# Performance work log

Hardware: AMD Instinct MI355X
Metric: run time of the kernel (lower is better)

## Reference

```python
import jax, jax.numpy as jnp
import numpy as np

ALPHA = 0.005
SCALE = 0.001
DELTA = 0.1
MAX_ITER = 50
EARLY = True


def setup_inputs() -> dict:
    key = jax.random.key(0)
    k1, k2, k3 = jax.random.split(key, 3)
    B, S, M, N = 32, 8, 512, 512
    x = jax.random.uniform(k1, (B, S, N), dtype=jnp.float32)
    A = jax.random.normal(k2, (B, S, M, N), dtype=jnp.float32) * 0.1
    b = jax.random.uniform(k3, (B, S, M), dtype=jnp.float32)
    return {"x": x, "A": A, "b": b}


def reference(x, A, b):
    # x: [B,S,N] primal iterate; A: [B,S,M,N] constraint matrices; b: [B,S,M]
    B, S = b.shape[0], b.shape[1]
    active0 = jnp.ones((B, S), dtype=bool)

    def body(carry, _):
        x_, active, stopped = carry
        # torch loop runs an iteration only while any(active) and not early-stopped
        run = jnp.any(active) & (~stopped)
        # Ax - b, clamped at 0 -> per-constraint violation
        Ax = jnp.einsum('bsn,bsmn->bsm', x_, A)          # [B,S,M]
        viol = jnp.clip(Ax - b, 0.0)
        new_active = jnp.sum(viol, axis=-1) >= DELTA      # ~(total < delta)
        stop_early = jnp.asarray(EARLY) & (~jnp.any(new_active))
        g = jnp.einsum('bsm,bsmn->bsn', viol, A)          # penalty gradient [B,S,N]
        lr = ALPHA / (1.0 + SCALE * g)
        x_upd = jnp.where(new_active[..., None], x_ - lr * g, x_)
        x_upd = jnp.clip(x_upd, 0.0)                      # clamp applied even to inactive rows
        # early stop happens BEFORE the update/clamp in the torch code
        x_new = jnp.where(stop_early, x_, x_upd)
        x_out = jnp.where(run, x_new, x_)
        active_out = jnp.where(run, new_active, active)
        stopped_out = stopped | (run & stop_early)
        return (x_out, active_out, stopped_out), None

    # torch: break when count > max_iter after increment -> up to max_iter+1 updates
    init = (x, active0, jnp.array(False))
    (x_final, _, _), _ = jax.lax.scan(body, init, None, length=MAX_ITER + 1)
    return x_final
```

## Files before the change

kernel.cpp:

```cpp
#include <hip/hip_runtime.h>

#define ALPHA 0.005f
#define SCALE 0.001f
#define DELTA 0.1f
#define MAXIT 51

constexpr int N = 512;
constexpr int M = 512;
constexpr int NTHREADS = 1024;
constexpr int NWAVES = NTHREADS / 64;
constexpr int MPW = M / NWAVES;
constexpr int NROWS = 256;
constexpr size_t WS_NEEDED = (size_t)NROWS * M * N * 2;

template<int CTRL>
__device__ __forceinline__ float dpp_mov(float v) {
    return __int_as_float(__builtin_amdgcn_update_dpp(
        0, __float_as_int(v), CTRL, 0xF, 0xF, true));
}

__device__ __forceinline__ float wave_sum_u(float d) {
    d += dpp_mov<0x111>(d);
    d += dpp_mov<0x112>(d);
    d += dpp_mov<0x114>(d);
    d += dpp_mov<0x118>(d);
    d += dpp_mov<0x142>(d);
    d += dpp_mov<0x143>(d);
    return __int_as_float(__builtin_amdgcn_readlane(__float_as_int(d), 63));
}

__device__ __forceinline__ float dot8(const float4& a, const float4& c,
                                      const float4& xa, const float4& xb) {
    return a.x*xa.x + a.y*xa.y + a.z*xa.z + a.w*xa.w
         + c.x*xb.x + c.y*xb.y + c.z*xb.z + c.w*xb.w;
}

__device__ __forceinline__ unsigned pack2_bf16(float f0, float f1) {
    unsigned a = __float_as_uint(f0); a += 0x7fffu + ((a >> 16) & 1u);
    unsigned b = __float_as_uint(f1); b += 0x7fffu + ((b >> 16) & 1u);
    return (a >> 16) | (b & 0xffff0000u);
}
__device__ __forceinline__ float bflo(unsigned u) { return __uint_as_float(u << 16); }
__device__ __forceinline__ float bfhi(unsigned u) { return __uint_as_float(u & 0xffff0000u); }

__device__ __forceinline__ void unpack4(uint2 u, float4& f) {
    f.x = bflo(u.x); f.y = bfhi(u.x); f.z = bflo(u.y); f.w = bfhi(u.y);
}

__global__ __launch_bounds__(NTHREADS, 4)
void lva_bf16_kernel(const float* __restrict__ x_in,
                     const float* __restrict__ A,
                     const float* __restrict__ bvec,
                     float* __restrict__ x_out,
                     unsigned short* __restrict__ wsA)
{
    __shared__ float b_lds[M];
    __shared__ float g_lds[2 * NWAVES * N];
    __shared__ float sv_lds[2 * NWAVES];
    __shared__ int bc_active;

    const int tid  = threadIdx.x;
    const int lane = tid & 63;
    const int w    = tid >> 6;
    const int r    = blockIdx.x;

    if (tid < M) b_lds[tid] = bvec[(size_t)r * M + tid];

    const int n0 = lane * 4;
    const int n1 = 256 + lane * 4;

    const float* xrow = x_in + (size_t)r * N;
    float4 xa = *(const float4*)(xrow + n0);
    float4 xb = *(const float4*)(xrow + n1);

    const float* Ablk = A + (size_t)r * M * N + (size_t)w * N;
    unsigned short* Wblk = wsA + (size_t)r * M * N + (size_t)w * N;

    __syncthreads();

    bool alive = true;

    {
        float4 ga = make_float4(0.f, 0.f, 0.f, 0.f);
        float4 gb = make_float4(0.f, 0.f, 0.f, 0.f);
        float sviol = 0.f;

        #pragma unroll 1
        for (int kk = 0; kk < MPW; kk += 4) {
            const float* p0 = Ablk + (size_t)(kk + 0) * (16 * N);
            const float* p1 = Ablk + (size_t)(kk + 1) * (16 * N);
            const float* p2 = Ablk + (size_t)(kk + 2) * (16 * N);
            const float* p3 = Ablk + (size_t)(kk + 3) * (16 * N);
            float4 a0 = *(const float4*)(p0 + n0), c0 = *(const float4*)(p0 + n1);
            float4 a1 = *(const float4*)(p1 + n0), c1 = *(const float4*)(p1 + n1);
            float4 a2 = *(const float4*)(p2 + n0), c2 = *(const float4*)(p2 + n1);
            float4 a3 = *(const float4*)(p3 + n0), c3 = *(const float4*)(p3 + n1);
            {
                unsigned short* q0 = Wblk + (size_t)(kk + 0) * (16 * N);
                unsigned short* q1 = Wblk + (size_t)(kk + 1) * (16 * N);
                unsigned short* q2 = Wblk + (size_t)(kk + 2) * (16 * N);
                unsigned short* q3 = Wblk + (size_t)(kk + 3) * (16 * N);
                *(uint2*)(q0 + n0) = make_uint2(pack2_bf16(a0.x, a0.y), pack2_bf16(a0.z, a0.w));
                *(uint2*)(q0 + n1) = make_uint2(pack2_bf16(c0.x, c0.y), pack2_bf16(c0.z, c0.w));
                *(uint2*)(q1 + n0) = make_uint2(pack2_bf16(a1.x, a1.y), pack2_bf16(a1.z, a1.w));
                *(uint2*)(q1 + n1) = make_uint2(pack2_bf16(c1.x, c1.y), pack2_bf16(c1.z, c1.w));
                *(uint2*)(q2 + n0) = make_uint2(pack2_bf16(a2.x, a2.y), pack2_bf16(a2.z, a2.w));
                *(uint2*)(q2 + n1) = make_uint2(pack2_bf16(c2.x, c2.y), pack2_bf16(c2.z, c2.w));
                *(uint2*)(q3 + n0) = make_uint2(pack2_bf16(a3.x, a3.y), pack2_bf16(a3.z, a3.w));
                *(uint2*)(q3 + n1) = make_uint2(pack2_bf16(c3.x, c3.y), pack2_bf16(c3.z, c3.w));
            }
            float bb0 = b_lds[w + 16 * (kk + 0)];
            float bb1 = b_lds[w + 16 * (kk + 1)];
            float bb2 = b_lds[w + 16 * (kk + 2)];
            float bb3 = b_lds[w + 16 * (kk + 3)];
            float d0 = wave_sum_u(dot8(a0, c0, xa, xb));
            float d1 = wave_sum_u(dot8(a1, c1, xa, xb));
            float d2 = wave_sum_u(dot8(a2, c2, xa, xb));
            float d3 = wave_sum_u(dot8(a3, c3, xa, xb));
            float v0 = fmaxf(d0 - bb0, 0.f);
            float v1 = fmaxf(d1 - bb1, 0.f);
            float v2 = fmaxf(d2 - bb2, 0.f);
            float v3 = fmaxf(d3 - bb3, 0.f);
            sviol += v0 + v1 + v2 + v3;
            ga.x += v0*a0.x + v1*a1.x + v2*a2.x + v3*a3.x;
            ga.y += v0*a0.y + v1*a1.y + v2*a2.y + v3*a3.y;
            ga.z += v0*a0.z + v1*a1.z + v2*a2.z + v3*a3.z;
            ga.w += v0*a0.w + v1*a1.w + v2*a2.w + v3*a3.w;
            gb.x += v0*c0.x + v1*c1.x + v2*c2.x + v3*c3.x;
            gb.y += v0*c0.y + v1*c1.y + v2*c2.y + v3*c3.y;
            gb.z += v0*c0.z + v1*c1.z + v2*c2.z + v3*c3.z;
            gb.w += v0*c0.w + v1*c1.w + v2*c2.w + v3*c3.w;
        }

        if (lane == 0) sv_lds[w] = sviol;
        *(float4*)(&g_lds[w * N + n0]) = ga;
        *(float4*)(&g_lds[w * N + n1]) = gb;
        __syncthreads();
        if (tid == 0) {
            float s = 0.f;
            #pragma unroll
            for (int i = 0; i < NWAVES; ++i) s += sv_lds[i];
            bc_active = (s >= DELTA) ? 1 : 0;
        }
        if (tid < N) {
            float s = 0.f;
            #pragma unroll
            for (int i = 0; i < NWAVES; ++i) s += g_lds[i * N + tid];
            g_lds[tid] = s;
        }
        __syncthreads();
        if (!bc_active) {
            alive = false;
        } else {
            float4 gfa = *(const float4*)(&g_lds[n0]);
            float4 gfb = *(const float4*)(&g_lds[n1]);
            xa.x = fmaxf(xa.x - (ALPHA / (1.f + SCALE*gfa.x)) * gfa.x, 0.f);
            xa.y = fmaxf(xa.y - (ALPHA / (1.f + SCALE*gfa.y)) * gfa.y, 0.f);
            xa.z = fmaxf(xa.z - (ALPHA / (1.f + SCALE*gfa.z)) * gfa.z, 0.f);
            xa.w = fmaxf(xa.w - (ALPHA / (1.f + SCALE*gfa.w)) * gfa.w, 0.f);
            xb.x = fmaxf(xb.x - (ALPHA / (1.f + SCALE*gfb.x)) * gfb.x, 0.f);
            xb.y = fmaxf(xb.y - (ALPHA / (1.f + SCALE*gfb.y)) * gfb.y, 0.f);
            xb.z = fmaxf(xb.z - (ALPHA / (1.f + SCALE*gfb.z)) * gfb.z, 0.f);
            xb.w = fmaxf(xb.w - (ALPHA / (1.f + SCALE*gfb.w)) * gfb.w, 0.f);
        }
    }

    const int h = lane >> 5;
    const int s = lane & 31;
    __syncthreads();
    if (w == 0) {
        *(float4*)(&g_lds[n0]) = xa;
        *(float4*)(&g_lds[n1]) = xb;
    }
    __syncthreads();
    float4 xf0 = *(const float4*)(&g_lds[  0 + s * 4]);
    float4 xf1 = *(const float4*)(&g_lds[128 + s * 4]);
    float4 xf2 = *(const float4*)(&g_lds[256 + s * 4]);
    float4 xf3 = *(const float4*)(&g_lds[384 + s * 4]);
    __syncthreads();

    if (alive) {
        const uint2* Wp = (const uint2*)(wsA + (size_t)r * M * N)
                          + (w + 16 * h) * 128 + s;
        const int mb = w + 16 * h;

        uint2 c0, c1, c2, c3, p0, p1, p2, p3;

        #define LOADG(b0, b1, b2, b3, Gn) do {  \
            b0 = Wp[(Gn) * 4096];               \
            b1 = Wp[(Gn) * 4096 + 32];          \
            b2 = Wp[(Gn) * 4096 + 64];          \
            b3 = Wp[(Gn) * 4096 + 96];          \
        } while (0)

        #define COMPUTE(b0, b1, b2, b3, G) do {                               \
            float4 f0, f1, f2, f3;                                            \
            unpack4(b0, f0); unpack4(b1, f1);                                 \
            unpack4(b2, f2); unpack4(b3, f3);                                 \
            float d = f0.x*xf0.x + f0.y*xf0.y + f0.z*xf0.z + f0.w*xf0.w       \
                    + f1.x*xf1.x + f1.y*xf1.y + f1.z*xf1.z + f1.w*xf1.w       \
                    + f2.x*xf2.x + f2.y*xf2.y + f2.z*xf2.z + f2.w*xf2.w       \
                    + f3.x*xf3.x + f3.y*xf3.y + f3.z*xf3.z + f3.w*xf3.w;      \
            d += dpp_mov<0xB1>(d);            \
            d += dpp_mov<0x4E>(d);            \
            d += dpp_mov<0x141>(d);           \
            d += dpp_mov<0x140>(d);           \
            d += __int_as_float(__builtin_amdgcn_ds_swizzle(                  \
                     __float_as_int(d), 0x401F));        \
            float v = fmaxf(d - b_lds[mb + 32 * (G)], 0.f);                   \
            sviol += v;                                                       \
            g0.x += v*f0.x; g0.y += v*f0.y; g0.z += v*f0.z; g0.w += v*f0.w;   \
            g1.x += v*f1.x; g1.y += v*f1.y; g1.z += v*f1.z; g1.w += v*f1.w;   \
            g2.x += v*f2.x; g2.y += v*f2.y; g2.z += v*f2.z; g2.w += v*f2.w;   \
            g3.x += v*f3.x; g3.y += v*f3.y; g3.z += v*f3.z; g3.w += v*f3.w;   \
        } while (0)

        LOADG(c0, c1, c2, c3, 0);

        for (int t = 1; t < MAXIT; ++t) {
            float4 g0 = make_float4(0.f, 0.f, 0.f, 0.f);
            float4 g1 = make_float4(0.f, 0.f, 0.f, 0.f);
            float4 g2 = make_float4(0.f, 0.f, 0.f, 0.f);
            float4 g3 = make_float4(0.f, 0.f, 0.f, 0.f);
            float sviol = 0.f;

            #pragma unroll 1
            for (int G = 0; G < 16; G += 2) {
                LOADG(p0, p1, p2, p3, G + 1);
                COMPUTE(c0, c1, c2, c3, G);
                LOADG(c0, c1, c2, c3, (G + 2) & 15);
                COMPUTE(p0, p1, p2, p3, G + 1);
            }

            if (s == 0) sv_lds[2 * w + h] = sviol;
            {
                const int gbase = (2 * w + h) * N + s * 4;
                *(float4*)(&g_lds[gbase +   0]) = g0;
                *(float4*)(&g_lds[gbase + 128]) = g1;
                *(float4*)(&g_lds[gbase + 256]) = g2;
                *(float4*)(&g_lds[gbase + 384]) = g3;
            }
            __syncthreads();
            if (tid == 0) {
                float sacc = 0.f;
                #pragma unroll
                for (int i = 0; i < 2 * NWAVES; ++i) sacc += sv_lds[i];
                bc_active = (sacc >= DELTA) ? 1 : 0;
            }
            if (tid < N) {
                float sacc = 0.f;
                #pragma unroll
                for (int i = 0; i < 2 * NWAVES; ++i) sacc += g_lds[i * N + tid];
                g_lds[tid] = sacc;
            }
            __syncthreads();
            if (!bc_active) break;

            float4 q0 = *(const float4*)(&g_lds[  0 + s * 4]);
            float4 q1 = *(const float4*)(&g_lds[128 + s * 4]);
            float4 q2 = *(const float4*)(&g_lds[256 + s * 4]);
            float4 q3 = *(const float4*)(&g_lds[384 + s * 4]);
            xf0.x = fmaxf(xf0.x - (ALPHA / (1.f + SCALE*q0.x)) * q0.x, 0.f);
            xf0.y = fmaxf(xf0.y - (ALPHA / (1.f + SCALE*q0.y)) * q0.y, 0.f);
            xf0.z = fmaxf(xf0.z - (ALPHA / (1.f + SCALE*q0.z)) * q0.z, 0.f);
            xf0.w = fmaxf(xf0.w - (ALPHA / (1.f + SCALE*q0.w)) * q0.w, 0.f);
            xf1.x = fmaxf(xf1.x - (ALPHA / (1.f + SCALE*q1.x)) * q1.x, 0.f);
            xf1.y = fmaxf(xf1.y - (ALPHA / (1.f + SCALE*q1.y)) * q1.y, 0.f);
            xf1.z = fmaxf(xf1.z - (ALPHA / (1.f + SCALE*q1.z)) * q1.z, 0.f);
            xf1.w = fmaxf(xf1.w - (ALPHA / (1.f + SCALE*q1.w)) * q1.w, 0.f);
            xf2.x = fmaxf(xf2.x - (ALPHA / (1.f + SCALE*q2.x)) * q2.x, 0.f);
            xf2.y = fmaxf(xf2.y - (ALPHA / (1.f + SCALE*q2.y)) * q2.y, 0.f);
            xf2.z = fmaxf(xf2.z - (ALPHA / (1.f + SCALE*q2.z)) * q2.z, 0.f);
            xf2.w = fmaxf(xf2.w - (ALPHA / (1.f + SCALE*q2.w)) * q2.w, 0.f);
            xf3.x = fmaxf(xf3.x - (ALPHA / (1.f + SCALE*q3.x)) * q3.x, 0.f);
            xf3.y = fmaxf(xf3.y - (ALPHA / (1.f + SCALE*q3.y)) * q3.y, 0.f);
            xf3.z = fmaxf(xf3.z - (ALPHA / (1.f + SCALE*q3.z)) * q3.z, 0.f);
            xf3.w = fmaxf(xf3.w - (ALPHA / (1.f + SCALE*q3.w)) * q3.w, 0.f);
            __syncthreads();
        }
        #undef LOADG
        #undef COMPUTE
    }

    if (w == 0 && h == 0) {
        float* orow = x_out + (size_t)r * N + s * 4;
        *(float4*)(orow +   0) = xf0;
        *(float4*)(orow + 128) = xf1;
        *(float4*)(orow + 256) = xf2;
        *(float4*)(orow + 384) = xf3;
    }
}

__global__ __launch_bounds__(NTHREADS, 4)
void lva_kernel(const float* __restrict__ x_in,
                const float* __restrict__ A,
                const float* __restrict__ bvec,
                float* __restrict__ x_out)
{
    __shared__ float b_lds[M];
    __shared__ float g_lds[NWAVES * N];
    __shared__ float sv_lds[NWAVES];
    __shared__ int bc_active;

    const int tid  = threadIdx.x;
    const int lane = tid & 63;
    const int w    = tid >> 6;
    const int r    = blockIdx.x;

    if (tid < M) b_lds[tid] = bvec[(size_t)r * M + tid];

    const int n0 = lane * 4;
    const int n1 = 256 + lane * 4;

    const float* xrow = x_in + (size_t)r * N;
    float4 xa = *(const float4*)(xrow + n0);
    float4 xb = *(const float4*)(xrow + n1);

    const float* Ablk = A + (size_t)r * M * N + (size_t)w * N;

    __syncthreads();

    for (int t = 0; t < MAXIT; ++t) {
        float4 ga = make_float4(0.f, 0.f, 0.f, 0.f);
        float4 gb = make_float4(0.f, 0.f, 0.f, 0.f);
        float sviol = 0.f;

        #pragma unroll 1
        for (int kk = 0; kk < MPW; kk += 4) {
            const float* p0 = Ablk + (size_t)(kk + 0) * (16 * N);
            const float* p1 = Ablk + (size_t)(kk + 1) * (16 * N);
            const float* p2 = Ablk + (size_t)(kk + 2) * (16 * N);
            const float* p3 = Ablk + (size_t)(kk + 3) * (16 * N);
            float4 a0 = *(const float4*)(p0 + n0), c0 = *(const float4*)(p0 + n1);
            float4 a1 = *(const float4*)(p1 + n0), c1 = *(const float4*)(p1 + n1);
            float4 a2 = *(const float4*)(p2 + n0), c2 = *(const float4*)(p2 + n1);
            float4 a3 = *(const float4*)(p3 + n0), c3 = *(const float4*)(p3 + n1);
            float bb0 = b_lds[w + 16 * (kk + 0)];
            float bb1 = b_lds[w + 16 * (kk + 1)];
            float bb2 = b_lds[w + 16 * (kk + 2)];
            float bb3 = b_lds[w + 16 * (kk + 3)];
            float d0 = wave_sum_u(dot8(a0, c0, xa, xb));
            float d1 = wave_sum_u(dot8(a1, c1, xa, xb));
            float d2 = wave_sum_u(dot8(a2, c2, xa, xb));
            float d3 = wave_sum_u(dot8(a3, c3, xa, xb));
            float v0 = fmaxf(d0 - bb0, 0.f);
            float v1 = fmaxf(d1 - bb1, 0.f);
            float v2 = fmaxf(d2 - bb2, 0.f);
            float v3 = fmaxf(d3 - bb3, 0.f);
            sviol += v0 + v1 + v2 + v3;
            ga.x += v0*a0.x + v1*a1.x + v2*a2.x + v3*a3.x;
            ga.y += v0*a0.y + v1*a1.y + v2*a2.y + v3*a3.y;
            ga.z += v0*a0.z + v1*a1.z + v2*a2.z + v3*a3.z;
            ga.w += v0*a0.w + v1*a1.w + v2*a2.w + v3*a3.w;
            gb.x += v0*c0.x + v1*c1.x + v2*c2.x + v3*c3.x;
            gb.y += v0*c0.y + v1*c1.y + v2*c2.y + v3*c3.y;
            gb.z += v0*c0.z + v1*c1.z + v2*c2.z + v3*c3.z;
            gb.w += v0*c0.w + v1*c1.w + v2*c2.w + v3*c3.w;
        }

        if (lane == 0) sv_lds[w] = sviol;
        *(float4*)(&g_lds[w * N + n0]) = ga;
        *(float4*)(&g_lds[w * N + n1]) = gb;
        __syncthreads();
        if (tid == 0) {
            float sacc = 0.f;
            #pragma unroll
            for (int i = 0; i < NWAVES; ++i) sacc += sv_lds[i];
            bc_active = (sacc >= DELTA) ? 1 : 0;
        }
        if (tid < N) {
            float sacc = 0.f;
            #pragma unroll
            for (int i = 0; i < NWAVES; ++i) sacc += g_lds[i * N + tid];
            g_lds[tid] = sacc;
        }
        __syncthreads();
        if (!bc_active) break;

        float4 gfa = *(const float4*)(&g_lds[n0]);
        float4 gfb = *(const float4*)(&g_lds[n1]);
        xa.x = fmaxf(xa.x - (ALPHA / (1.f + SCALE*gfa.x)) * gfa.x, 0.f);
        xa.y = fmaxf(xa.y - (ALPHA / (1.f + SCALE*gfa.y)) * gfa.y, 0.f);
        xa.z = fmaxf(xa.z - (ALPHA / (1.f + SCALE*gfa.z)) * gfa.z, 0.f);
        xa.w = fmaxf(xa.w - (ALPHA / (1.f + SCALE*gfa.w)) * gfa.w, 0.f);
        xb.x = fmaxf(xb.x - (ALPHA / (1.f + SCALE*gfb.x)) * gfb.x, 0.f);
        xb.y = fmaxf(xb.y - (ALPHA / (1.f + SCALE*gfb.y)) * gfb.y, 0.f);
        xb.z = fmaxf(xb.z - (ALPHA / (1.f + SCALE*gfb.z)) * gfb.z, 0.f);
        xb.w = fmaxf(xb.w - (ALPHA / (1.f + SCALE*gfb.w)) * gfb.w, 0.f);
        __syncthreads();
    }

    float* orow = x_out + (size_t)r * N;
    if (w == 0) {
        *(float4*)(orow + n0) = xa;
        *(float4*)(orow + n1) = xb;
    }
}

extern "C" void kernel_launch(void* const* d_in, const int* in_sizes, int n_in,
                              void* d_out, int out_size, void* d_ws, size_t ws_size,
                              hipStream_t stream)
{
    const float* x  = (const float*)d_in[0];
    const float* A  = (const float*)d_in[1];
    const float* b  = (const float*)d_in[2];
    float* out      = (float*)d_out;

    if (ws_size >= WS_NEEDED) {
        lva_bf16_kernel<<<dim3(NROWS), dim3(NTHREADS), 0, stream>>>(
            x, A, b, out, (unsigned short*)d_ws);
    } else {
        lva_kernel<<<dim3(NROWS), dim3(NTHREADS), 0, stream>>>(x, A, b, out);
    }
}
```

Measured before the change: 1.323 ms.

## Cache tail rows of bf16 A in LDS and widen iteration loads

The last 96 constraint rows of each block's bf16 copy of A now live in shared memory instead of the global workspace, so each iteration reads 13 of 16 row groups from global and 3 from LDS. The per-lane layout moves to 8 contiguous elements so rows load as uint4 instead of uint2. The loop is fully unrolled with a 4-deep register prefetch that crosses iterations. The two half-wave gradient partials are merged with ds_bpermute before the block reduction, halving the g_lds reduction work. The aim is less global and L2 traffic and latency per iteration, at the cost of about 96KB of LDS and more registers, which may reduce occupancy.

```diff
diff --git a/kernel.cpp b/kernel.cpp
--- a/kernel.cpp
+++ b/kernel.cpp
@@ -12,6 +12,9 @@
 constexpr int MPW = M / NWAVES;
 constexpr int NROWS = 256;
 constexpr size_t WS_NEEDED = (size_t)NROWS * M * N * 2;
+
+constexpr int CACHE_M0 = 416;
+constexpr int CACHE_KK0 = 26;
 
 template<int CTRL>
 __device__ __forceinline__ float dpp_mov(float v) {
@@ -43,10 +46,6 @@
 __device__ __forceinline__ float bflo(unsigned u) { return __uint_as_float(u << 16); }
 __device__ __forceinline__ float bfhi(unsigned u) { return __uint_as_float(u & 0xffff0000u); }
 
-__device__ __forceinline__ void unpack4(uint2 u, float4& f) {
-    f.x = bflo(u.x); f.y = bfhi(u.x); f.z = bflo(u.y); f.w = bfhi(u.y);
-}
-
 __global__ __launch_bounds__(NTHREADS, 4)
 void lva_bf16_kernel(const float* __restrict__ x_in,
                      const float* __restrict__ A,
@@ -54,10 +53,11 @@
                      float* __restrict__ x_out,
                      unsigned short* __restrict__ wsA)
 {
-    __shared__ float b_lds[M];
-    __shared__ float g_lds[2 * NWAVES * N];
-    __shared__ float sv_lds[2 * NWAVES];
+    __shared__ __align__(16) float b_lds[M];
+    __shared__ __align__(16) float g_lds[NWAVES * N];
+    __shared__ float sv_lds[NWAVES];
     __shared__ int bc_active;
+    __shared__ __align__(16) uint2 A_lds[96 * 128];
 
     const int tid  = threadIdx.x;
     const int lane = tid & 63;
@@ -84,6 +84,22 @@
         float4 ga = make_float4(0.f, 0.f, 0.f, 0.f);
         float4 gb = make_float4(0.f, 0.f, 0.f, 0.f);
         float sviol = 0.f;
+
+        #define STROW(j, aj, cj) do {                                               \
+            if (kk + (j) >= CACHE_KK0) {                                            \
+                const int rl = w + 16 * (kk + (j)) - CACHE_M0;                      \
+                A_lds[rl * 128 + lane]      = make_uint2(pack2_bf16(aj.x, aj.y),    \
+                                                         pack2_bf16(aj.z, aj.w));   \
+                A_lds[rl * 128 + 64 + lane] = make_uint2(pack2_bf16(cj.x, cj.y),    \
+                                                         pack2_bf16(cj.z, cj.w));   \
+            } else {                                                                \
+                unsigned short* q = Wblk + (size_t)(kk + (j)) * (16 * N);           \
+                *(uint2*)(q + n0) = make_uint2(pack2_bf16(aj.x, aj.y),              \
+                                               pack2_bf16(aj.z, aj.w));             \
+                *(uint2*)(q + n1) = make_uint2(pack2_bf16(cj.x, cj.y),              \
+                                               pack2_bf16(cj.z, cj.w));             \
+            }                                                                       \
+        } while (0)
 
         #pragma unroll 1
         for (int kk = 0; kk < MPW; kk += 4) {
@@ -95,20 +111,7 @@
             float4 a1 = *(const float4*)(p1 + n0), c1 = *(const float4*)(p1 + n1);
             float4 a2 = *(const float4*)(p2 + n0), c2 = *(const float4*)(p2 + n1);
             float4 a3 = *(const float4*)(p3 + n0), c3 = *(const float4*)(p3 + n1);
-            {
-                unsigned short* q0 = Wblk + (size_t)(kk + 0) * (16 * N);
-                unsigned short* q1 = Wblk + (size_t)(kk + 1) * (16 * N);
-                unsigned short* q2 = Wblk + (size_t)(kk + 2) * (16 * N);
-                unsigned short* q3 = Wblk + (size_t)(kk + 3) * (16 * N);
-                *(uint2*)(q0 + n0) = make_uint2(pack2_bf16(a0.x, a0.y), pack2_bf16(a0.z, a0.w));
-                *(uint2*)(q0 + n1) = make_uint2(pack2_bf16(c0.x, c0.y), pack2_bf16(c0.z, c0.w));
-                *(uint2*)(q1 + n0) = make_uint2(pack2_bf16(a1.x, a1.y), pack2_bf16(a1.z, a1.w));
-                *(uint2*)(q1 + n1) = make_uint2(pack2_bf16(c1.x, c1.y), pack2_bf16(c1.z, c1.w));
-                *(uint2*)(q2 + n0) = make_uint2(pack2_bf16(a2.x, a2.y), pack2_bf16(a2.z, a2.w));
-                *(uint2*)(q2 + n1) = make_uint2(pack2_bf16(c2.x, c2.y), pack2_bf16(c2.z, c2.w));
-                *(uint2*)(q3 + n0) = make_uint2(pack2_bf16(a3.x, a3.y), pack2_bf16(a3.z, a3.w));
-                *(uint2*)(q3 + n1) = make_uint2(pack2_bf16(c3.x, c3.y), pack2_bf16(c3.z, c3.w));
-            }
+            STROW(0, a0, c0); STROW(1, a1, c1); STROW(2, a2, c2); STROW(3, a3, c3);
             float bb0 = b_lds[w + 16 * (kk + 0)];
             float bb1 = b_lds[w + 16 * (kk + 1)];
             float bb2 = b_lds[w + 16 * (kk + 2)];
@@ -131,6 +134,7 @@
             gb.z += v0*c0.z + v1*c1.z + v2*c2.z + v3*c3.z;
             gb.w += v0*c0.w + v1*c1.w + v2*c2.w + v3*c3.w;
         }
+        #undef STROW
 
         if (lane == 0) sv_lds[w] = sviol;
         *(float4*)(&g_lds[w * N + n0]) = ga;
@@ -173,50 +177,56 @@
         *(float4*)(&g_lds[n1]) = xb;
     }
     __syncthreads();
-    float4 xf0 = *(const float4*)(&g_lds[  0 + s * 4]);
-    float4 xf1 = *(const float4*)(&g_lds[128 + s * 4]);
-    float4 xf2 = *(const float4*)(&g_lds[256 + s * 4]);
-    float4 xf3 = *(const float4*)(&g_lds[384 + s * 4]);
+    float4 xf0 = *(const float4*)(&g_lds[      8 * s    ]);
+    float4 xf1 = *(const float4*)(&g_lds[      8 * s + 4]);
+    float4 xf2 = *(const float4*)(&g_lds[256 + 8 * s    ]);
+    float4 xf3 = *(const float4*)(&g_lds[256 + 8 * s + 4]);
     __syncthreads();
 
     if (alive) {
-        const uint2* Wp = (const uint2*)(wsA + (size_t)r * M * N)
-                          + (w + 16 * h) * 128 + s;
+        const uint4* Wp4 = (const uint4*)(wsA + (size_t)r * M * N)
+                           + (w + 16 * h) * 64 + s;
         const int mb = w + 16 * h;
-
-        uint2 c0, c1, c2, c3, p0, p1, p2, p3;
-
-        #define LOADG(b0, b1, b2, b3, Gn) do {  \
-            b0 = Wp[(Gn) * 4096];               \
-            b1 = Wp[(Gn) * 4096 + 32];          \
-            b2 = Wp[(Gn) * 4096 + 64];          \
-            b3 = Wp[(Gn) * 4096 + 96];          \
+        const int xadr = (lane ^ 32) << 2;
+
+        uint4 b0a, b0b, b1a, b1b, b2a, b2b, b3a, b3b;
+
+        #define LOADG4(pa, pb, Gc) do {          \
+            pa = Wp4[(Gc) * 2048];               \
+            pb = Wp4[(Gc) * 2048 + 32];          \
         } while (0)
 
-        #define COMPUTE(b0, b1, b2, b3, G) do {                               \
-            float4 f0, f1, f2, f3;                                            \
-            unpack4(b0, f0); unpack4(b1, f1);                                 \
-            unpack4(b2, f2); unpack4(b3, f3);                                 \
-            float d = f0.x*xf0.x + f0.y*xf0.y + f0.z*xf0.z + f0.w*xf0.w       \
-                    + f1.x*xf1.x + f1.y*xf1.y + f1.z*xf1.z + f1.w*xf1.w       \
-                    + f2.x*xf2.x + f2.y*xf2.y + f2.z*xf2.z + f2.w*xf2.w       \
-                    + f3.x*xf3.x + f3.y*xf3.y + f3.z*xf3.z + f3.w*xf3.w;      \
-            d += dpp_mov<0xB1>(d);            \
-            d += dpp_mov<0x4E>(d);            \
-            d += dpp_mov<0x141>(d);           \
-            d += dpp_mov<0x140>(d);           \
-            d += __int_as_float(__builtin_amdgcn_ds_swizzle(                  \
-                     __float_as_int(d), 0x401F));        \
-            float v = fmaxf(d - b_lds[mb + 32 * (G)], 0.f);                   \
-            sviol += v;                                                       \
-            g0.x += v*f0.x; g0.y += v*f0.y; g0.z += v*f0.z; g0.w += v*f0.w;   \
-            g1.x += v*f1.x; g1.y += v*f1.y; g1.z += v*f1.z; g1.w += v*f1.w;   \
-            g2.x += v*f2.x; g2.y += v*f2.y; g2.z += v*f2.z; g2.w += v*f2.w;   \
-            g3.x += v*f3.x; g3.y += v*f3.y; g3.z += v*f3.z; g3.w += v*f3.w;   \
+        #define CORE(pa, pb, Gc) do {                                              \
+            float4 f0, f1, f2, f3;                                                 \
+            f0.x = bflo(pa.x); f0.y = bfhi(pa.x); f0.z = bflo(pa.y); f0.w = bfhi(pa.y); \
+            f1.x = bflo(pa.z); f1.y = bfhi(pa.z); f1.z = bflo(pa.w); f1.w = bfhi(pa.w); \
+            f2.x = bflo(pb.x); f2.y = bfhi(pb.x); f2.z = bflo(pb.y); f2.w = bfhi(pb.y); \
+            f3.x = bflo(pb.z); f3.y = bfhi(pb.z); f3.z = bflo(pb.w); f3.w = bfhi(pb.w); \
+            float d = f0.x*xf0.x + f0.y*xf0.y + f0.z*xf0.z + f0.w*xf0.w            \
+                    + f1.x*xf1.x + f1.y*xf1.y + f1.z*xf1.z + f1.w*xf1.w            \
+                    + f2.x*xf2.x + f2.y*xf2.y + f2.z*xf2.z + f2.w*xf2.w            \
+                    + f3.x*xf3.x + f3.y*xf3.y + f3.z*xf3.z + f3.w*xf3.w;           \
+            d += dpp_mov<0xB1>(d);                 \
+            d += dpp_mov<0x4E>(d);                 \
+            d += dpp_mov<0x141>(d);                \
+            d += dpp_mov<0x140>(d);                \
+            d += __int_as_float(__builtin_amdgcn_ds_swizzle(                       \
+                     __float_as_int(d), 0x401F));             \
+            float v = fmaxf(d - b_lds[mb + 32 * (Gc)], 0.f);                       \
+            sviol += v;                                                            \
+            g0.x += v*f0.x; g0.y += v*f0.y; g0.z += v*f0.z; g0.w += v*f0.w;        \
+            g1.x += v*f1.x; g1.y += v*f1.y; g1.z += v*f1.z; g1.w += v*f1.w;        \
+            g2.x += v*f2.x; g2.y += v*f2.y; g2.z += v*f2.z; g2.w += v*f2.w;        \
+            g3.x += v*f3.x; g3.y += v*f3.y; g3.z += v*f3.z; g3.w += v*f3.w;        \
         } while (0)
 
-        LOADG(c0, c1, c2, c3, 0);
-
+        #define MRG(x) (x) += __int_as_float(                                      \
+            __builtin_amdgcn_ds_bpermute(xadr, __float_as_int(x)))
+
+        LOADG4(b0a, b0b, 0); LOADG4(b1a, b1b, 1);
+        LOADG4(b2a, b2b, 2); LOADG4(b3a, b3b, 3);
+
+        #pragma unroll 1
         for (int t = 1; t < MAXIT; ++t) {
             float4 g0 = make_float4(0.f, 0.f, 0.f, 0.f);
             float4 g1 = make_float4(0.f, 0.f, 0.f, 0.f);
@@ -224,42 +234,72 @@
             float4 g3 = make_float4(0.f, 0.f, 0.f, 0.f);
             float sviol = 0.f;
 
-            #pragma unroll 1
-            for (int G = 0; G < 16; G += 2) {
-                LOADG(p0, p1, p2, p3, G + 1);
-                COMPUTE(c0, c1, c2, c3, G);
-                LOADG(c0, c1, c2, c3, (G + 2) & 15);
-                COMPUTE(p0, p1, p2, p3, G + 1);
-            }
-
-            if (s == 0) sv_lds[2 * w + h] = sviol;
+            CORE(b0a, b0b,  0);  LOADG4(b0a, b0b,  4);
+            CORE(b1a, b1b,  1);  LOADG4(b1a, b1b,  5);
+            CORE(b2a, b2b,  2);  LOADG4(b2a, b2b,  6);
+            CORE(b3a, b3b,  3);  LOADG4(b3a, b3b,  7);
+            CORE(b0a, b0b,  4);  LOADG4(b0a, b0b,  8);
+            CORE(b1a, b1b,  5);  LOADG4(b1a, b1b,  9);
+            CORE(b2a, b2b,  6);  LOADG4(b2a, b2b, 10);
+            CORE(b3a, b3b,  7);  LOADG4(b3a, b3b, 11);
+            CORE(b0a, b0b,  8);  LOADG4(b0a, b0b, 12);
+            CORE(b1a, b1b,  9);
+            CORE(b2a, b2b, 10);
+            CORE(b3a, b3b, 11);
+            CORE(b0a, b0b, 12);
+            LOADG4(b0a, b0b, 0); LOADG4(b1a, b1b, 1);
+            LOADG4(b2a, b2b, 2); LOADG4(b3a, b3b, 3);
+
             {
-                const int gbase = (2 * w + h) * N + s * 4;
-                *(float4*)(&g_lds[gbase +   0]) = g0;
-                *(float4*)(&g_lds[gbase + 128]) = g1;
-                *(float4*)(&g_lds[gbase + 256]) = g2;
-                *(float4*)(&g_lds[gbase + 384]) = g3;
+                uint4 la = *(const uint4*)&A_lds[(mb +  0) * 128 + 2 * s];
+                uint4 lb = *(const uint4*)&A_lds[(mb +  0) * 128 + 64 + 2 * s];
+                CORE(la, lb, 13);
+            }
+            {
+                uint4 la = *(const uint4*)&A_lds[(mb + 32) * 128 + 2 * s];
+                uint4 lb = *(const uint4*)&A_lds[(mb + 32) * 128 + 64 + 2 * s];
+                CORE(la, lb, 14);
+            }
+            {
+                uint4 la = *(const uint4*)&A_lds[(mb + 64) * 128 + 2 * s];
+                uint4 lb = *(const uint4*)&A_lds[(mb + 64) * 128 + 64 + 2 * s];
+                CORE(la, lb, 15);
+            }
+
+            MRG(g0.x); MRG(g0.y); MRG(g0.z); MRG(g0.w);
+            MRG(g1.x); MRG(g1.y); MRG(g1.z); MRG(g1.w);
+            MRG(g2.x); MRG(g2.y); MRG(g2.z); MRG(g2.w);
+            MRG(g3.x); MRG(g3.y); MRG(g3.z); MRG(g3.w);
+            MRG(sviol);
+
+            if (h == 0) {
+                const int gb = w * N + 8 * s;
+                *(float4*)(&g_lds[gb      ]) = g0;
+                *(float4*)(&g_lds[gb +   4]) = g1;
+                *(float4*)(&g_lds[gb + 256]) = g2;
+                *(float4*)(&g_lds[gb + 260]) = g3;
+                if (s == 0) sv_lds[w] = sviol;
             }
             __syncthreads();
             if (tid == 0) {
                 float sacc = 0.f;
                 #pragma unroll
-                for (int i = 0; i < 2 * NWAVES; ++i) sacc += sv_lds[i];
+                for (int i = 0; i < NWAVES; ++i) sacc += sv_lds[i];
                 bc_active = (sacc >= DELTA) ? 1 : 0;
             }
             if (tid < N) {
                 float sacc = 0.f;
                 #pragma unroll
-                for (int i = 0; i < 2 * NWAVES; ++i) sacc += g_lds[i * N + tid];
+                for (int i = 0; i < NWAVES; ++i) sacc += g_lds[i * N + tid];
                 g_lds[tid] = sacc;
             }
             __syncthreads();
             if (!bc_active) break;
 
-            float4 q0 = *(const float4*)(&g_lds[  0 + s * 4]);
-            float4 q1 = *(const float4*)(&g_lds[128 + s * 4]);
-            float4 q2 = *(const float4*)(&g_lds[256 + s * 4]);
-            float4 q3 = *(const float4*)(&g_lds[384 + s * 4]);
+            float4 q0 = *(const float4*)(&g_lds[      8 * s    ]);
+            float4 q1 = *(const float4*)(&g_lds[      8 * s + 4]);
+            float4 q2 = *(const float4*)(&g_lds[256 + 8 * s    ]);
+            float4 q3 = *(const float4*)(&g_lds[256 + 8 * s + 4]);
             xf0.x = fmaxf(xf0.x - (ALPHA / (1.f + SCALE*q0.x)) * q0.x, 0.f);
             xf0.y = fmaxf(xf0.y - (ALPHA / (1.f + SCALE*q0.y)) * q0.y, 0.f);
             xf0.z = fmaxf(xf0.z - (ALPHA / (1.f + SCALE*q0.z)) * q0.z, 0.f);
@@ -278,16 +318,17 @@
             xf3.w = fmaxf(xf3.w - (ALPHA / (1.f + SCALE*q3.w)) * q3.w, 0.f);
             __syncthreads();
         }
-        #undef LOADG
-        #undef COMPUTE
+        #undef LOADG4
+        #undef CORE
+        #undef MRG
     }
 
     if (w == 0 && h == 0) {
-        float* orow = x_out + (size_t)r * N + s * 4;
-        *(float4*)(orow +   0) = xf0;
-        *(float4*)(orow + 128) = xf1;
-        *(float4*)(orow + 256) = xf2;
-        *(float4*)(orow + 384) = xf3;
+        float* orow = x_out + (size_t)r * N;
+        *(float4*)(orow +       8 * s    ) = xf0;
+        *(float4*)(orow +       8 * s + 4) = xf1;
+        *(float4*)(orow + 256 + 8 * s    ) = xf2;
+        *(float4*)(orow + 256 + 8 * s + 4) = xf3;
     }
 }
 
```

Measured after the change: 4.709 ms. 3.56x slower.

## Cache last 96 constraint rows of A in LDS and merge half-wave partials via bpermute

Applied to the files above, without the earlier changes.

During the first pass, rows 416 to 511 of the bf16 copy of A are written to a 96KB LDS buffer instead of the global workspace. Each later iteration then reads 13 of its 16 row groups from global memory and 3 from LDS, cutting per-iteration global and L2 traffic. The two half-wave partial gradients are combined with ds_bpermute before the LDS reduction, which halves the g_lds scratch and the reduction loop length. The larger LDS footprint limits how many blocks can share a CU and changes the software pipelining at the boundary between global and LDS row groups.

```diff
diff --git a/kernel.cpp b/kernel.cpp
--- a/kernel.cpp
+++ b/kernel.cpp
@@ -12,6 +12,9 @@
 constexpr int MPW = M / NWAVES;
 constexpr int NROWS = 256;
 constexpr size_t WS_NEEDED = (size_t)NROWS * M * N * 2;
+
+constexpr int CACHE_M0 = 416;
+constexpr int CACHE_KK0 = 26;
 
 template<int CTRL>
 __device__ __forceinline__ float dpp_mov(float v) {
@@ -54,10 +57,11 @@
                      float* __restrict__ x_out,
                      unsigned short* __restrict__ wsA)
 {
-    __shared__ float b_lds[M];
-    __shared__ float g_lds[2 * NWAVES * N];
-    __shared__ float sv_lds[2 * NWAVES];
+    __shared__ __align__(16) float b_lds[M];
+    __shared__ __align__(16) float g_lds[NWAVES * N];
+    __shared__ float sv_lds[NWAVES];
     __shared__ int bc_active;
+    __shared__ __align__(16) uint2 A_lds[96 * 128];
 
     const int tid  = threadIdx.x;
     const int lane = tid & 63;
@@ -84,6 +88,22 @@
         float4 ga = make_float4(0.f, 0.f, 0.f, 0.f);
         float4 gb = make_float4(0.f, 0.f, 0.f, 0.f);
         float sviol = 0.f;
+
+        #define STROW(j, aj, cj) do {                                               \
+            if (kk + (j) >= CACHE_KK0) {                                            \
+                const int rl = w + 16 * (kk + (j)) - CACHE_M0;                      \
+                A_lds[rl * 128 + lane]      = make_uint2(pack2_bf16(aj.x, aj.y),    \
+                                                         pack2_bf16(aj.z, aj.w));   \
+                A_lds[rl * 128 + 64 + lane] = make_uint2(pack2_bf16(cj.x, cj.y),    \
+                                                         pack2_bf16(cj.z, cj.w));   \
+            } else {                                                                \
+                unsigned short* q = Wblk + (size_t)(kk + (j)) * (16 * N);           \
+                *(uint2*)(q + n0) = make_uint2(pack2_bf16(aj.x, aj.y),              \
+                                               pack2_bf16(aj.z, aj.w));             \
+                *(uint2*)(q + n1) = make_uint2(pack2_bf16(cj.x, cj.y),              \
+                                               pack2_bf16(cj.z, cj.w));             \
+            }                                                                       \
+        } while (0)
 
         #pragma unroll 1
         for (int kk = 0; kk < MPW; kk += 4) {
@@ -95,20 +115,7 @@
             float4 a1 = *(const float4*)(p1 + n0), c1 = *(const float4*)(p1 + n1);
             float4 a2 = *(const float4*)(p2 + n0), c2 = *(const float4*)(p2 + n1);
             float4 a3 = *(const float4*)(p3 + n0), c3 = *(const float4*)(p3 + n1);
-            {
-                unsigned short* q0 = Wblk + (size_t)(kk + 0) * (16 * N);
-                unsigned short* q1 = Wblk + (size_t)(kk + 1) * (16 * N);
-                unsigned short* q2 = Wblk + (size_t)(kk + 2) * (16 * N);
-                unsigned short* q3 = Wblk + (size_t)(kk + 3) * (16 * N);
-                *(uint2*)(q0 + n0) = make_uint2(pack2_bf16(a0.x, a0.y), pack2_bf16(a0.z, a0.w));
-                *(uint2*)(q0 + n1) = make_uint2(pack2_bf16(c0.x, c0.y), pack2_bf16(c0.z, c0.w));
-                *(uint2*)(q1 + n0) = make_uint2(pack2_bf16(a1.x, a1.y), pack2_bf16(a1.z, a1.w));
-                *(uint2*)(q1 + n1) = make_uint2(pack2_bf16(c1.x, c1.y), pack2_bf16(c1.z, c1.w));
-                *(uint2*)(q2 + n0) = make_uint2(pack2_bf16(a2.x, a2.y), pack2_bf16(a2.z, a2.w));
-                *(uint2*)(q2 + n1) = make_uint2(pack2_bf16(c2.x, c2.y), pack2_bf16(c2.z, c2.w));
-                *(uint2*)(q3 + n0) = make_uint2(pack2_bf16(a3.x, a3.y), pack2_bf16(a3.z, a3.w));
-                *(uint2*)(q3 + n1) = make_uint2(pack2_bf16(c3.x, c3.y), pack2_bf16(c3.z, c3.w));
-            }
+            STROW(0, a0, c0); STROW(1, a1, c1); STROW(2, a2, c2); STROW(3, a3, c3);
             float bb0 = b_lds[w + 16 * (kk + 0)];
             float bb1 = b_lds[w + 16 * (kk + 1)];
             float bb2 = b_lds[w + 16 * (kk + 2)];
@@ -131,6 +138,7 @@
             gb.z += v0*c0.z + v1*c1.z + v2*c2.z + v3*c3.z;
             gb.w += v0*c0.w + v1*c1.w + v2*c2.w + v3*c3.w;
         }
+        #undef STROW
 
         if (lane == 0) sv_lds[w] = sviol;
         *(float4*)(&g_lds[w * N + n0]) = ga;
@@ -183,6 +191,7 @@
         const uint2* Wp = (const uint2*)(wsA + (size_t)r * M * N)
                           + (w + 16 * h) * 128 + s;
         const int mb = w + 16 * h;
+        const int xadr = (lane ^ 32) << 2;
 
         uint2 c0, c1, c2, c3, p0, p1, p2, p3;
 
@@ -215,8 +224,12 @@
             g3.x += v*f3.x; g3.y += v*f3.y; g3.z += v*f3.z; g3.w += v*f3.w;   \
         } while (0)
 
+        #define MRG(x) (x) += __int_as_float(                                 \
+            __builtin_amdgcn_ds_bpermute(xadr, __float_as_int(x)))
+
         LOADG(c0, c1, c2, c3, 0);
 
+        #pragma unroll 1
         for (int t = 1; t < MAXIT; ++t) {
             float4 g0 = make_float4(0.f, 0.f, 0.f, 0.f);
             float4 g1 = make_float4(0.f, 0.f, 0.f, 0.f);
@@ -225,32 +238,59 @@
             float sviol = 0.f;
 
             #pragma unroll 1
-            for (int G = 0; G < 16; G += 2) {
+            for (int G = 0; G < 12; G += 2) {
                 LOADG(p0, p1, p2, p3, G + 1);
                 COMPUTE(c0, c1, c2, c3, G);
-                LOADG(c0, c1, c2, c3, (G + 2) & 15);
+                LOADG(c0, c1, c2, c3, G + 2);
                 COMPUTE(p0, p1, p2, p3, G + 1);
             }
-
-            if (s == 0) sv_lds[2 * w + h] = sviol;
+            COMPUTE(c0, c1, c2, c3, 12);
+            LOADG(c0, c1, c2, c3, 0);
+
             {
-                const int gbase = (2 * w + h) * N + s * 4;
-                *(float4*)(&g_lds[gbase +   0]) = g0;
-                *(float4*)(&g_lds[gbase + 128]) = g1;
-                *(float4*)(&g_lds[gbase + 256]) = g2;
-                *(float4*)(&g_lds[gbase + 384]) = g3;
+                const int base = mb * 128 + s;
+                p0 = A_lds[base]; p1 = A_lds[base + 32];
+                p2 = A_lds[base + 64]; p3 = A_lds[base + 96];
+                COMPUTE(p0, p1, p2, p3, 13);
+            }
+            {
+                const int base = (mb + 32) * 128 + s;
+                p0 = A_lds[base]; p1 = A_lds[base + 32];
+                p2 = A_lds[base + 64]; p3 = A_lds[base + 96];
+                COMPUTE(p0, p1, p2, p3, 14);
+            }
+            {
+                const int base = (mb + 64) * 128 + s;
+                p0 = A_lds[base]; p1 = A_lds[base + 32];
+                p2 = A_lds[base + 64]; p3 = A_lds[base + 96];
+                COMPUTE(p0, p1, p2, p3, 15);
+            }
+
+            MRG(g0.x); MRG(g0.y); MRG(g0.z); MRG(g0.w);
+            MRG(g1.x); MRG(g1.y); MRG(g1.z); MRG(g1.w);
+            MRG(g2.x); MRG(g2.y); MRG(g2.z); MRG(g2.w);
+            MRG(g3.x); MRG(g3.y); MRG(g3.z); MRG(g3.w);
+            MRG(sviol);
+
+            if (h == 0) {
+                const int gb = w * N + s * 4;
+                *(float4*)(&g_lds[gb      ]) = g0;
+                *(float4*)(&g_lds[gb + 128]) = g1;
+                *(float4*)(&g_lds[gb + 256]) = g2;
+                *(float4*)(&g_lds[gb + 384]) = g3;
+                if (s == 0) sv_lds[w] = sviol;
             }
             __syncthreads();
             if (tid == 0) {
                 float sacc = 0.f;
                 #pragma unroll
-                for (int i = 0; i < 2 * NWAVES; ++i) sacc += sv_lds[i];
+                for (int i = 0; i < NWAVES; ++i) sacc += sv_lds[i];
                 bc_active = (sacc >= DELTA) ? 1 : 0;
             }
             if (tid < N) {
                 float sacc = 0.f;
                 #pragma unroll
-                for (int i = 0; i < 2 * NWAVES; ++i) sacc += g_lds[i * N + tid];
+                for (int i = 0; i < NWAVES; ++i) sacc += g_lds[i * N + tid];
                 g_lds[tid] = sacc;
             }
             __syncthreads();
@@ -280,6 +320,7 @@
         }
         #undef LOADG
         #undef COMPUTE
+        #undef MRG
     }
 
     if (w == 0 && h == 0) {
```

Measured after the change: 1.146 ms, median of 2. 13.4% less time.
